# Optimization experiments

Measured on AMD Instinct MI355X. Metric: run time of the kernel, lower is better.

The kernel has to match this reference:

```python
import jax, jax.numpy as jnp
import numpy as np

X, Y, Q, DOWNSAMPLE, HID, OUT = 2048, 2048, 32, 2, 32, 1
Xd, Yd = X // DOWNSAMPLE, Y // DOWNSAMPLE
N = X * Y


def _make_grid():
    # Faithful port of FeatureXY.__init__ buffer construction (torch linspace/meshgrid ij).
    xs = np.linspace(0.5 / X, 1 - 0.5 / X, X, dtype=np.float32)
    ys = np.linspace(0.5 / Y, 1 - 0.5 / Y, Y, dtype=np.float32)
    xv, yv = np.meshgrid(xs, ys, indexing='ij')  # [X, Y]
    xy = np.stack((xv.ravel(), yv.ravel()), axis=1)  # [N, 2] columns (x, y)
    xy = xy * np.array([Xd, Yd], dtype=np.float32)
    integer = xy.astype(np.int64)  # positive -> trunc == floor, matches .long()
    decimal = xy - integer.astype(np.float32)
    x0 = np.clip(integer[:, 0], 0, Xd - 1).astype(np.int32)
    y0 = np.clip(integer[:, 1], 0, Yd - 1).astype(np.int32)
    x1 = np.minimum(x0 + 1, Xd - 1).astype(np.int32)
    y1 = np.minimum(y0 + 1, Yd - 1).astype(np.int32)
    wx = decimal[:, 0:1].astype(np.float32)
    wy = decimal[:, 1:2].astype(np.float32)
    return x0, y0, x1, y1, wx, wy


def setup_inputs() -> dict:
    key = jax.random.key(0)
    k = jax.random.split(key, 8)
    x0, y0, x1, y1, wx, wy = _make_grid()
    M = 0.0002 * jax.random.uniform(k[0], (Yd, Xd, Q), dtype=jnp.float32) - 0.0001
    s1 = 1.0 / np.sqrt(Q)
    s2 = 1.0 / np.sqrt(HID)
    return {
        'M': M,
        'x0': jnp.asarray(x0), 'y0': jnp.asarray(y0),
        'x1': jnp.asarray(x1), 'y1': jnp.asarray(y1),
        'wx': jnp.asarray(wx), 'wy': jnp.asarray(wy),
        'W1': jax.random.normal(k[1], (Q, HID), jnp.float32) * s1,
        'b1': jax.random.normal(k[2], (HID,), jnp.float32) * s1,
        'W2': jax.random.normal(k[3], (HID, HID), jnp.float32) * s2,
        'b2': jax.random.normal(k[4], (HID,), jnp.float32) * s2,
        'W3': jax.random.normal(k[5], (HID, OUT), jnp.float32) * s2,
        'b3': jax.random.normal(k[6], (OUT,), jnp.float32) * s2,
    }


def reference(M, x0, y0, x1, y1, wx, wy, W1, b1, W2, b2, W3, b3):
    # Bilinear gather of features: [N, Q]
    f = (M[y0, x0] * (1.0 - wx) * (1.0 - wy)
         + M[y0, x1] * wx * (1.0 - wy)
         + M[y1, x0] * (1.0 - wx) * wy
         + M[y1, x1] * wx * wy)
    # Tiny render MLP (Linear -> ReLU -> Linear -> ReLU -> Linear)
    h = jax.nn.relu(f @ W1 + b1)
    h = jax.nn.relu(h @ W2 + b2)
    return h @ W3 + b3  # [N, 1]
```

## Files before the change

kernel.cpp:

```cpp
#include <hip/hip_runtime.h>
#include <hip/hip_bf16.h>

#define XD 1024
#define NPTS (2048 * 2048)

typedef short  short8 __attribute__((ext_vector_type(8)));
typedef float  f32x4  __attribute__((ext_vector_type(4)));

static __device__ __forceinline__ short f2bf(float x) {
    __hip_bfloat16 b = __float2bfloat16(x);
    return *reinterpret_cast<const short*>(&b);
}

__global__ __launch_bounds__(256, 3) void RenderXY_kernel(
    const float* __restrict__ M,
    const float* __restrict__ W1, const float* __restrict__ b1,
    const float* __restrict__ W2, const float* __restrict__ b2,
    const float* __restrict__ W3, const float* __restrict__ b3,
    float* __restrict__ out)
{
    const int lane = threadIdx.x & 63;
    const int l15  = lane & 15;
    const int hi   = lane >> 4;
    const int waveId = (blockIdx.x << 2) | (threadIdx.x >> 6);

    short8 w1f0, w1f1, w2f0, w2f1;
#pragma unroll
    for (int j = 0; j < 8; ++j) {
        const int k1 = 8 * hi + j;
        w1f0[j] = f2bf(W1[k1 * 32 + l15]);
        w1f1[j] = f2bf(W1[k1 * 32 + 16 + l15]);
        const int k2 = 16 * (j >> 2) + 4 * hi + (j & 3);
        w2f0[j] = f2bf(W2[k2 * 32 + l15]);
        w2f1[j] = f2bf(W2[k2 * 32 + 16 + l15]);
    }
    f32x4 c10, c11, c20, c21;
#pragma unroll
    for (int r = 0; r < 4; ++r) {
        c10[r] = b1[4 * hi + r];
        c11[r] = b1[16 + 4 * hi + r];
        c20[r] = b2[4 * hi + r];
        c21[r] = b2[16 + 4 * hi + r];
    }
    float w3a[4], w3b[4];
#pragma unroll
    for (int r = 0; r < 4; ++r) { w3a[r] = W3[4 * hi + r]; w3b[r] = W3[16 + 4 * hi + r]; }
    const float bias3 = b3[0];

    for (int it = 0; it < 16; ++it) {
        const int nb  = (waveId + (it << 12)) << 6;
        const int   px  = nb >> 11;
        const int   x0  = px >> 1;
        const int   x1  = min(x0 + 1, XD - 1);
        const float wx  = (px & 1) ? 0.75f : 0.25f;
        const float iwx = 1.0f - wx;
        const int   pyb = nb & 2047;
        const int   colA = x0 * 32 + 8 * hi;
        const int   colB = x1 * 32 + 8 * hi;

        float ot[4];
#pragma unroll
        for (int t = 0; t < 4; ++t) {
            const int   py = pyb + t * 16 + l15;
            const int   y0 = py >> 1;
            const int   y1 = min(y0 + 1, XD - 1);
            const float wy  = (py & 1) ? 0.75f : 0.25f;
            const float iwy = 1.0f - wy;
            const float w00 = iwx * iwy, w01 = wx * iwy;
            const float w10 = iwx * wy,  w11 = wx * wy;

            const float* pr0 = M + (size_t)y0 * (XD * 32);
            const float* pr1 = M + (size_t)y1 * (XD * 32);
            const float4 a0 = *(const float4*)(pr0 + colA);
            const float4 a1 = *(const float4*)(pr0 + colA + 4);
            const float4 b0 = *(const float4*)(pr0 + colB);
            const float4 b1v = *(const float4*)(pr0 + colB + 4);
            const float4 c0 = *(const float4*)(pr1 + colA);
            const float4 c1 = *(const float4*)(pr1 + colA + 4);
            const float4 d0 = *(const float4*)(pr1 + colB);
            const float4 d1 = *(const float4*)(pr1 + colB + 4);

            short8 bq;
            bq[0] = f2bf(fmaf(d0.x, w11, fmaf(c0.x, w10, fmaf(b0.x, w01, a0.x * w00))));
            bq[1] = f2bf(fmaf(d0.y, w11, fmaf(c0.y, w10, fmaf(b0.y, w01, a0.y * w00))));
            bq[2] = f2bf(fmaf(d0.z, w11, fmaf(c0.z, w10, fmaf(b0.z, w01, a0.z * w00))));
            bq[3] = f2bf(fmaf(d0.w, w11, fmaf(c0.w, w10, fmaf(b0.w, w01, a0.w * w00))));
            bq[4] = f2bf(fmaf(d1.x, w11, fmaf(c1.x, w10, fmaf(b1v.x, w01, a1.x * w00))));
            bq[5] = f2bf(fmaf(d1.y, w11, fmaf(c1.y, w10, fmaf(b1v.y, w01, a1.y * w00))));
            bq[6] = f2bf(fmaf(d1.z, w11, fmaf(c1.z, w10, fmaf(b1v.z, w01, a1.z * w00))));
            bq[7] = f2bf(fmaf(d1.w, w11, fmaf(c1.w, w10, fmaf(b1v.w, w01, a1.w * w00))));

            f32x4 h0 = __builtin_amdgcn_mfma_f32_16x16x32_bf16(w1f0, bq, c10, 0, 0, 0);
            f32x4 h1 = __builtin_amdgcn_mfma_f32_16x16x32_bf16(w1f1, bq, c11, 0, 0, 0);

            short8 hb;
            hb[0] = f2bf(fmaxf(h0[0], 0.0f));
            hb[1] = f2bf(fmaxf(h0[1], 0.0f));
            hb[2] = f2bf(fmaxf(h0[2], 0.0f));
            hb[3] = f2bf(fmaxf(h0[3], 0.0f));
            hb[4] = f2bf(fmaxf(h1[0], 0.0f));
            hb[5] = f2bf(fmaxf(h1[1], 0.0f));
            hb[6] = f2bf(fmaxf(h1[2], 0.0f));
            hb[7] = f2bf(fmaxf(h1[3], 0.0f));

            f32x4 e0 = __builtin_amdgcn_mfma_f32_16x16x32_bf16(w2f0, hb, c20, 0, 0, 0);
            f32x4 e1 = __builtin_amdgcn_mfma_f32_16x16x32_bf16(w2f1, hb, c21, 0, 0, 0);

            float p = 0.0f;
#pragma unroll
            for (int r = 0; r < 4; ++r) {
                p = fmaf(fmaxf(e0[r], 0.0f), w3a[r], p);
                p = fmaf(fmaxf(e1[r], 0.0f), w3b[r], p);
            }
            p += __shfl_xor(p, 16, 64);
            p += __shfl_xor(p, 32, 64);
            ot[t] = p;
        }

        const float osel = (hi == 0) ? ot[0] : (hi == 1) ? ot[1] : (hi == 2) ? ot[2] : ot[3];
        out[nb + (hi << 4) + l15] = osel + bias3;
    }
}

extern "C" void kernel_launch(void* const* d_in, const int* in_sizes, int n_in,
                              void* d_out, int out_size, void* d_ws, size_t ws_size,
                              hipStream_t stream) {
    const float* M  = (const float*)d_in[0];
    const float* W1 = (const float*)d_in[7];
    const float* b1 = (const float*)d_in[8];
    const float* W2 = (const float*)d_in[9];
    const float* b2 = (const float*)d_in[10];
    const float* W3 = (const float*)d_in[11];
    const float* b3 = (const float*)d_in[12];
    float* out = (float*)d_out;

    hipLaunchKernelGGL(RenderXY_kernel, dim3(1024), dim3(256), 0, stream,
                       M, W1, b1, W2, b2, W3, b3, out);
}
```

Before: 346.2 us.

## Stage x-interpolated feature rows in LDS and reuse across y samples

Each wave now loads the 33 needed source rows once, blends them along x, stores them as bf16 in per-wave LDS, and then does the y blend from LDS for each output point. This cuts the redundant global gathers, which fetched four corners per point with heavy overlap between neighbouring points. It adds an extra bf16 rounding of the x-interpolated value and LDS traffic. Occupancy hint is raised from 3 to 4 blocks. There is no barrier between the LDS write and read, which relies on a wave only touching its own region.

```diff
diff --git a/kernel.cpp b/kernel.cpp
--- a/kernel.cpp
+++ b/kernel.cpp
@@ -3,6 +3,7 @@
 
 #define XD 1024
 #define NPTS (2048 * 2048)
+#define PITCH 40
 
 typedef short  short8 __attribute__((ext_vector_type(8)));
 typedef float  f32x4  __attribute__((ext_vector_type(4)));
@@ -11,8 +12,11 @@
     __hip_bfloat16 b = __float2bfloat16(x);
     return *reinterpret_cast<const short*>(&b);
 }
+static __device__ __forceinline__ float bf2f(short s) {
+    return __uint_as_float(((unsigned)(unsigned short)s) << 16);
+}
 
-__global__ __launch_bounds__(256, 3) void RenderXY_kernel(
+__global__ __launch_bounds__(256, 4) void RenderXY_kernel(
     const float* __restrict__ M,
     const float* __restrict__ W1, const float* __restrict__ b1,
     const float* __restrict__ W2, const float* __restrict__ b2,
@@ -22,7 +26,11 @@
     const int lane = threadIdx.x & 63;
     const int l15  = lane & 15;
     const int hi   = lane >> 4;
-    const int waveId = (blockIdx.x << 2) | (threadIdx.x >> 6);
+    const int wid  = threadIdx.x >> 6;
+    const int waveId = (blockIdx.x << 2) | wid;
+
+    __shared__ short lds_all[4][33 * PITCH + 8];
+    short* myr = &lds_all[wid][0];
 
     short8 w1f0, w1f1, w2f0, w2f1;
 #pragma unroll
@@ -47,48 +55,55 @@
     for (int r = 0; r < 4; ++r) { w3a[r] = W3[4 * hi + r]; w3b[r] = W3[16 + 4 * hi + r]; }
     const float bias3 = b3[0];
 
+    const int srow = lane >> 2;
+    const int ss   = lane & 3;
+
     for (int it = 0; it < 16; ++it) {
         const int nb  = (waveId + (it << 12)) << 6;
         const int   px  = nb >> 11;
         const int   x0  = px >> 1;
         const int   x1  = min(x0 + 1, XD - 1);
         const float wx  = (px & 1) ? 0.75f : 0.25f;
-        const float iwx = 1.0f - wx;
         const int   pyb = nb & 2047;
-        const int   colA = x0 * 32 + 8 * hi;
-        const int   colB = x1 * 32 + 8 * hi;
+        const int   Y0  = pyb >> 1;
+
+#pragma unroll
+        for (int p = 0; p < 3; ++p) {
+            const int row = p * 16 + srow;
+            const int rc  = min(Y0 + row, XD - 1);
+            const float* pr = M + (size_t)rc * (XD * 32);
+            const float4 va  = *(const float4*)(pr + x0 * 32 + ss * 8);
+            const float4 va2 = *(const float4*)(pr + x0 * 32 + ss * 8 + 4);
+            const float4 vb  = *(const float4*)(pr + x1 * 32 + ss * 8);
+            const float4 vb2 = *(const float4*)(pr + x1 * 32 + ss * 8 + 4);
+            short8 rb;
+            rb[0] = f2bf(fmaf(wx, vb.x  - va.x,  va.x));
+            rb[1] = f2bf(fmaf(wx, vb.y  - va.y,  va.y));
+            rb[2] = f2bf(fmaf(wx, vb.z  - va.z,  va.z));
+            rb[3] = f2bf(fmaf(wx, vb.w  - va.w,  va.w));
+            rb[4] = f2bf(fmaf(wx, vb2.x - va2.x, va2.x));
+            rb[5] = f2bf(fmaf(wx, vb2.y - va2.y, va2.y));
+            rb[6] = f2bf(fmaf(wx, vb2.z - va2.z, va2.z));
+            rb[7] = f2bf(fmaf(wx, vb2.w - va2.w, va2.w));
+            if (row <= 32)
+                *(short8*)(myr + row * PITCH + ss * 8) = rb;
+        }
 
         float ot[4];
 #pragma unroll
         for (int t = 0; t < 4; ++t) {
-            const int   py = pyb + t * 16 + l15;
-            const int   y0 = py >> 1;
-            const int   y1 = min(y0 + 1, XD - 1);
-            const float wy  = (py & 1) ? 0.75f : 0.25f;
-            const float iwy = 1.0f - wy;
-            const float w00 = iwx * iwy, w01 = wx * iwy;
-            const float w10 = iwx * wy,  w11 = wx * wy;
-
-            const float* pr0 = M + (size_t)y0 * (XD * 32);
-            const float* pr1 = M + (size_t)y1 * (XD * 32);
-            const float4 a0 = *(const float4*)(pr0 + colA);
-            const float4 a1 = *(const float4*)(pr0 + colA + 4);
-            const float4 b0 = *(const float4*)(pr0 + colB);
-            const float4 b1v = *(const float4*)(pr0 + colB + 4);
-            const float4 c0 = *(const float4*)(pr1 + colA);
-            const float4 c1 = *(const float4*)(pr1 + colA + 4);
-            const float4 d0 = *(const float4*)(pr1 + colB);
-            const float4 d1 = *(const float4*)(pr1 + colB + 4);
+            const int   k0 = t * 8 + (l15 >> 1);
+            const float wy = (l15 & 1) ? 0.75f : 0.25f;
+            const short8 r0 = *(const short8*)(myr + k0 * PITCH + hi * 8);
+            const short8 r1 = *(const short8*)(myr + (k0 + 1) * PITCH + hi * 8);
 
             short8 bq;
-            bq[0] = f2bf(fmaf(d0.x, w11, fmaf(c0.x, w10, fmaf(b0.x, w01, a0.x * w00))));
-            bq[1] = f2bf(fmaf(d0.y, w11, fmaf(c0.y, w10, fmaf(b0.y, w01, a0.y * w00))));
-            bq[2] = f2bf(fmaf(d0.z, w11, fmaf(c0.z, w10, fmaf(b0.z, w01, a0.z * w00))));
-            bq[3] = f2bf(fmaf(d0.w, w11, fmaf(c0.w, w10, fmaf(b0.w, w01, a0.w * w00))));
-            bq[4] = f2bf(fmaf(d1.x, w11, fmaf(c1.x, w10, fmaf(b1v.x, w01, a1.x * w00))));
-            bq[5] = f2bf(fmaf(d1.y, w11, fmaf(c1.y, w10, fmaf(b1v.y, w01, a1.y * w00))));
-            bq[6] = f2bf(fmaf(d1.z, w11, fmaf(c1.z, w10, fmaf(b1v.z, w01, a1.z * w00))));
-            bq[7] = f2bf(fmaf(d1.w, w11, fmaf(c1.w, w10, fmaf(b1v.w, w01, a1.w * w00))));
+#pragma unroll
+            for (int j = 0; j < 8; ++j) {
+                const float af = bf2f(r0[j]);
+                const float bf_ = bf2f(r1[j]);
+                bq[j] = f2bf(fmaf(wy, bf_ - af, af));
+            }
 
             f32x4 h0 = __builtin_amdgcn_mfma_f32_16x16x32_bf16(w1f0, bq, c10, 0, 0, 0);
             f32x4 h1 = __builtin_amdgcn_mfma_f32_16x16x32_bf16(w1f1, bq, c11, 0, 0, 0);
```

Result: faster. 282.4 us (-18.4%).
